# Optimization experiments

Hardware: AMD Instinct MI355X
Metric: run time of the kernel (lower is better)

The kernel has to match this reference:

```python
import jax, jax.numpy as jnp
import numpy as np

NB = 10          # number_of_basis (hardcoded in module)
MAX_RADIUS = 3.5
DIM_SH = 16      # spherical harmonics l = 0..3 -> (3+1)^2 components


def spherical_harmonics_l3(vec):
    # real spherical harmonics l=0..3 of the normalized vector,
    # 'component' normalization (each component has unit variance on S^2)
    r = jnp.sqrt(jnp.sum(vec * vec, -1, keepdims=True))
    u = vec / jnp.maximum(r, 1e-9)
    x, y, z = u[..., 0], u[..., 1], u[..., 2]
    s3, s5, s15 = jnp.sqrt(3.0), jnp.sqrt(5.0), jnp.sqrt(15.0)
    c358 = jnp.sqrt(35.0 / 8.0); c218 = jnp.sqrt(21.0 / 8.0)
    sh = [jnp.ones_like(x),
          s3 * x, s3 * y, s3 * z,
          s15 * x * y, s15 * y * z, (s5 / 2) * (3 * z * z - 1),
          s15 * x * z, (s15 / 2) * (x * x - y * y),
          c358 * y * (3 * x * x - y * y), jnp.sqrt(105.0) * x * y * z,
          c218 * y * (5 * z * z - 1), (jnp.sqrt(7.0) / 2) * z * (5 * z * z - 3),
          c218 * x * (5 * z * z - 1), (jnp.sqrt(105.0) / 2) * z * (x * x - y * y),
          c358 * x * (x * x - 3 * y * y)]
    return jnp.stack(sh, -1)  # [E, 16]


def soft_one_hot(r):
    # e3nn soft_one_hot_linspace, basis='smooth_finite', cutoff=True
    values = jnp.linspace(0.0, MAX_RADIUS, NB + 2)[1:-1]
    step = MAX_RADIUS / (NB + 1)
    u = (r[:, None] - values) / step
    mask = jnp.abs(u) < 1.0
    us = jnp.where(mask, u, 0.0)
    y = jnp.where(mask, jnp.exp(-1.0 / (1.0 - us * us)), 0.0)
    return 1.14136 * jnp.exp(2.0) * y * jnp.sqrt(float(NB))  # * number_of_basis**0.5


def soft_unit_step(t):
    ts = jnp.where(t > 0, t, 1.0)
    return jnp.where(t > 0, jnp.exp(-1.0 / ts), 0.0)


def fcnet(e, W1, W2):
    # e3nn FullyConnectedNet([10, 16, weight_numel], act=silu): bias-free,
    # fan-in normalized linear layers
    h = jax.nn.silu(e @ W1 / jnp.sqrt(float(e.shape[-1])))
    return h @ W2 / jnp.sqrt(float(W1.shape[-1]))


def setup_inputs() -> dict:
    key = jax.random.key(0)
    ks = jax.random.split(key, 9)
    N, E, C, DK = 20000, 50000, 16, 8
    pos = jax.random.uniform(ks[0], (N, 3), jnp.float32) * 2.0  # box so most edges < max_radius
    x = jax.random.normal(ks[1], (N, C), jnp.float32)
    Wq = jax.random.normal(ks[2], (C, DK), jnp.float32)
    Wk1 = jax.random.normal(ks[3], (NB, 16), jnp.float32)
    Wk2 = jax.random.normal(ks[4], (16, C * DIM_SH * DK), jnp.float32)
    Wv1 = jax.random.normal(ks[5], (NB, 16), jnp.float32)
    Wv2 = jax.random.normal(ks[6], (16, C * DIM_SH * DK), jnp.float32)
    edge_src = jax.random.randint(ks[7], (E,), 0, N, jnp.int32)
    edge_dst = jax.random.randint(ks[8], (E,), 0, N, jnp.int32)
    return {"pos": pos, "x": x, "Wq": Wq, "Wk1": Wk1, "Wk2": Wk2,
            "Wv1": Wv1, "Wv2": Wv2, "edge_src": edge_src, "edge_dst": edge_dst}


def reference(pos, x, Wq, Wk1, Wk2, Wv1, Wv2, edge_src, edge_dst):
    N, C = x.shape
    E = edge_src.shape[0]
    DK = Wq.shape[1]
    edge_vec = pos[edge_src] - pos[edge_dst]                    # [E, 3]
    r = jnp.sqrt(jnp.sum(edge_vec * edge_vec, -1) + 1e-18)      # [E]
    emb = soft_one_hot(r)                                       # [E, 10]
    cutoff = soft_unit_step(10.0 * (1.0 - r / MAX_RADIUS))      # [E]
    sh = spherical_harmonics_l3(edge_vec)                       # [E, 16]
    # per-edge weight-conditioned tensor products (shared_weights=False)
    wk = fcnet(emb, Wk1, Wk2).reshape(E, C, DIM_SH, DK)
    wv = fcnet(emb, Wv1, Wv2).reshape(E, C, DIM_SH, DK)
    xs = x[edge_src]                                            # gather [E, C]
    norm = jnp.sqrt(float(C * DIM_SH))
    k = jnp.einsum('ec,ej,ecjo->eo', xs, sh, wk) / norm         # [E, DK]
    v = jnp.einsum('ec,ej,ecjo->eo', xs, sh, wv) / norm         # [E, DK]
    q = x @ Wq                                                  # [N, DK]
    logits = jnp.sum(q[edge_dst] * k, -1) / jnp.sqrt(float(DK)) # [E]
    expv = cutoff * jnp.exp(logits)
    z = jax.ops.segment_sum(expv, edge_dst, num_segments=N)     # segment-softmax denom
    z = jnp.where(z == 0.0, 1.0, z)
    alpha = expv / z[edge_dst]
    w = jnp.sqrt(jax.nn.relu(alpha))
    out = jax.ops.segment_sum(w[:, None] * v, edge_dst, num_segments=N)  # [N, DK]
    return out
```

## Files before the change

### kernel.cpp

```cpp
#include <hip/hip_runtime.h>
#include <hip/hip_bf16.h>

#define NBASIS 10
#define CDIM 16
#define DKDIM 8
#define JDIM 16

typedef _Float16 half8 __attribute__((ext_vector_type(8)));
typedef _Float16 half4 __attribute__((ext_vector_type(4)));
typedef float floatx4 __attribute__((ext_vector_type(4)));

__device__ __forceinline__ float ldf(const void* p, int i, int f32) {
    if (f32) return ((const float*)p)[i];
    return __bfloat162float(((const __hip_bfloat16*)p)[i]);
}

__device__ __forceinline__ int detect_f32(const void* x) {
    unsigned short b = ((const unsigned short*)x)[threadIdx.x & 63];
    float v = __uint_as_float(((unsigned int)b) << 16);
    bool bad = !(fabsf(v) < 1000.0f) || (v != 0.0f && fabsf(v) < 1e-15f);
    unsigned long long m = __ballot(bad);
    return (__popcll(m) >= 8) ? 1 : 0;
}

__device__ __forceinline__ const float* uniform_ptr(const float* p) {
    uint64_t v = (uint64_t)p;
    uint32_t lo = __builtin_amdgcn_readfirstlane((uint32_t)v);
    uint32_t hi = __builtin_amdgcn_readfirstlane((uint32_t)(v >> 32));
    return (const float*)(((uint64_t)hi << 32) | lo);
}

__global__ __launch_bounds__(256) void prep_kernel(
    const void* __restrict__ x, const void* __restrict__ Wq,
    const void* __restrict__ Wk1, const void* __restrict__ Wk2,
    const void* __restrict__ Wv1, const void* __restrict__ Wv2,
    float* __restrict__ w1k, float* __restrict__ w1v,
    float* __restrict__ qbuf, float* __restrict__ zbuf,
    float* __restrict__ outacc, _Float16* __restrict__ Bpk, int N)
{
    const int f32 = detect_f32(x);
    int i = blockIdx.x * 256 + threadIdx.x;
    if (i < 160) { w1k[i] = ldf(Wk1, i, f32); w1v[i] = ldf(Wv1, i, f32); }
    if (i < 65536) {
        int j = i & 7, lane = (i >> 3) & 63, ks = (i >> 9) & 7, nt = i >> 12;
        int kk = ks * 32 + (lane >> 4) * 8 + j;
        int nn = nt * 16 + (lane & 15);
        int c = kk >> 4, jj = kk & 15;
        int net = nn >> 7, m = (nn >> 3) & 15, o = nn & 7;
        float v = ldf(net ? Wv2 : Wk2, m * 2048 + c * 128 + jj * 8 + o, f32);
        Bpk[i] = (_Float16)v;
    }
    if (i < N) {
        zbuf[i] = 0.0f;
        float xr[CDIM];
        #pragma unroll
        for (int c = 0; c < CDIM; ++c) xr[c] = ldf(x, i * CDIM + c, f32);
        #pragma unroll
        for (int o = 0; o < DKDIM; ++o) {
            float acc = 0.0f;
            #pragma unroll
            for (int c = 0; c < CDIM; ++c)
                acc = fmaf(xr[c], ldf(Wq, c * DKDIM + o, f32), acc);
            qbuf[i * DKDIM + o] = acc;
        }
    }
    if (i < N * 8) outacc[i] = 0.0f;
}

__global__ __launch_bounds__(256) void edge_kernel(
    const void* __restrict__ pos, const void* __restrict__ x,
    const int* __restrict__ esrc, const int* __restrict__ edst,
    const float* __restrict__ w1k, const float* __restrict__ w1v,
    const float* __restrict__ qbuf, const _Float16* __restrict__ Bpk,
    float* __restrict__ zbuf, float* __restrict__ outacc, int E)
{
    __shared__ union {
        struct { float xs[64][17]; float sh[64][17]; } g;
        _Float16 A[16384];
        struct { float pk[2][64][9]; float pv[2][64][9]; } p;
    } u;
    __shared__ _Float16 hm16[2][16][64];
    __shared__ float cut_lds[64];
    __shared__ float evs_lds[64];
    __shared__ int   d_lds[64];

    const int f32  = detect_f32(x);
    const int tid  = threadIdx.x;
    const int lane = tid & 63;
    const int w    = tid >> 6;
    const int q    = lane >> 4;
    const int e0   = blockIdx.x * 64;
    const int e_g  = e0 + lane;
    const int eidx = (e_g < E) ? e_g : (E - 1);
    const int s = esrc[eidx], d = edst[eidx];

    float vx = ldf(pos, s * 3 + 0, f32) - ldf(pos, d * 3 + 0, f32);
    float vy = ldf(pos, s * 3 + 1, f32) - ldf(pos, d * 3 + 1, f32);
    float vz = ldf(pos, s * 3 + 2, f32) - ldf(pos, d * 3 + 2, f32);
    float r2 = vx * vx + vy * vy + vz * vz;
    float r  = sqrtf(r2 + 1e-18f);

    if (w == 0) {
        float rsh = sqrtf(r2);
        float inv = 1.0f / fmaxf(rsh, 1e-9f);
        float ux = vx * inv, uy = vy * inv, uz = vz * inv;
        const float s3   = 1.7320508075688772f;
        const float s5   = 2.23606797749979f;
        const float s15  = 3.872983346207417f;
        const float c358 = 2.091650066335189f;
        const float c218 = 1.6201851746019651f;
        const float s105 = 10.246950765959598f;
        const float s7h  = 1.3228756555322954f;
        float xx = ux * ux, yy = uy * uy, zz = uz * uz;
        float sh[16];
        sh[0] = 1.0f;
        sh[1] = s3 * ux; sh[2] = s3 * uy; sh[3] = s3 * uz;
        sh[4] = s15 * ux * uy;
        sh[5] = s15 * uy * uz;
        sh[6] = 0.5f * s5 * (3.0f * zz - 1.0f);
        sh[7] = s15 * ux * uz;
        sh[8] = 0.5f * s15 * (xx - yy);
        sh[9] = c358 * uy * (3.0f * xx - yy);
        sh[10] = s105 * ux * uy * uz;
        sh[11] = c218 * uy * (5.0f * zz - 1.0f);
        sh[12] = s7h * uz * (5.0f * zz - 3.0f);
        sh[13] = c218 * ux * (5.0f * zz - 1.0f);
        sh[14] = 0.5f * s105 * uz * (xx - yy);
        sh[15] = c358 * ux * (xx - 3.0f * yy);
        #pragma unroll
        for (int j = 0; j < 16; ++j) u.g.sh[lane][j] = sh[j];
        float tcut = 10.0f * (1.0f - r * (1.0f / 3.5f));
        cut_lds[lane] = (tcut > 0.0f) ? expf(-1.0f / tcut) : 0.0f;
        d_lds[lane] = d;
    } else if (w == 1) {
        #pragma unroll
        for (int c = 0; c < CDIM; ++c)
            u.g.xs[lane][c] = ldf(x, s * CDIM + c, f32);
    } else {
        const float* w1 = uniform_ptr((w == 2) ? w1k : w1v);
        const int net = w - 2;
        float emb[NBASIS];
        const float step = 3.5f / 11.0f;
        const float istep = 11.0f / 3.5f;
        const float coef = (float)(1.14136 * 7.38905609893065 * 3.1622776601683795);
        #pragma unroll
        for (int i = 0; i < NBASIS; ++i) {
            float uu = (r - step * (float)(i + 1)) * istep; uu *= uu;
            emb[i] = (uu < 1.0f) ? coef * expf(-1.0f / (1.0f - uu)) : 0.0f;
        }
        const float inv_s10 = 0.31622776601683794f;
        #pragma unroll
        for (int m = 0; m < 16; ++m) {
            float pre = 0.0f;
            #pragma unroll
            for (int nb = 0; nb < NBASIS; ++nb)
                pre = fmaf(emb[nb], w1[nb * 16 + m], pre);
            pre *= inv_s10;
            hm16[net][m][lane] = (_Float16)(pre / (1.0f + expf(-pre)));
        }
    }
    __syncthreads();

    half8 af[8];
    {
        const int erow = w * 16 + (lane & 15);
        const int coff = q >> 1, jj0 = (q & 1) * 8;
        #pragma unroll
        for (int ks = 0; ks < 8; ++ks) {
            float xsv = u.g.xs[erow][ks * 2 + coff];
            half8 a;
            #pragma unroll
            for (int j = 0; j < 8; ++j)
                a[j] = (_Float16)(xsv * u.g.sh[erow][jj0 + j]);
            af[ks] = a;
        }
    }
    __syncthreads();
    {
        half8* Af = (half8*)u.A;
        #pragma unroll
        for (int ks = 0; ks < 8; ++ks)
            Af[(w * 8 + ks) * 64 + lane] = af[ks];
    }
    __syncthreads();

    float part[16];
    #pragma unroll
    for (int i = 0; i < 16; ++i) part[i] = 0.0f;
    const int b3  = (lane >> 3) & 1;
    const int net = w >> 1;
    const half8* Af = (const half8*)u.A;
    const half8* Bf = (const half8*)Bpk;

    #pragma unroll
    for (int l = 0; l < 4; ++l) {
        const int nt = 4 * w + l;
        floatx4 acc[4];
        #pragma unroll
        for (int rt = 0; rt < 4; ++rt) acc[rt] = (floatx4){0.f, 0.f, 0.f, 0.f};
        #pragma unroll
        for (int ks = 0; ks < 8; ++ks) {
            half8 b = Bf[(nt * 8 + ks) * 64 + lane];
            #pragma unroll
            for (int rt = 0; rt < 4; ++rt) {
                half8 a = Af[(rt * 8 + ks) * 64 + lane];
                acc[rt] = __builtin_amdgcn_mfma_f32_16x16x32_f16(a, b, acc[rt], 0, 0, 0);
            }
        }
        const int m = (2 * nt + b3) & 15;
        #pragma unroll
        for (int rt = 0; rt < 4; ++rt) {
            half4 hv = *(const half4*)&hm16[net][m][rt * 16 + q * 4];
            #pragma unroll
            for (int rr = 0; rr < 4; ++rr)
                part[rt * 4 + rr] = fmaf((float)hv[rr], acc[rt][rr], part[rt * 4 + rr]);
        }
    }
    #pragma unroll
    for (int i = 0; i < 16; ++i) part[i] += __shfl_xor(part[i], 8, 64);

    __syncthreads();
    if (b3 == 0) {
        const int o = lane & 7;
        #pragma unroll
        for (int i = 0; i < 16; ++i) {
            const int e = (i >> 2) * 16 + q * 4 + (i & 3);
            if (w < 2) u.p.pk[w][e][o] = part[i];
            else       u.p.pv[w - 2][e][o] = part[i];
        }
    }
    __syncthreads();

    if (tid < 64) {
        const int dd = d_lds[tid];
        float logit = 0.0f;
        #pragma unroll
        for (int o = 0; o < 8; ++o) {
            float kv = u.p.pk[0][tid][o] + u.p.pk[1][tid][o];
            logit = fmaf(qbuf[(size_t)dd * 8 + o], kv, logit);
        }
        logit *= (1.0f / 64.0f) * 0.35355339059327373f;
        float ev = cut_lds[tid] * expf(logit);
        if (e0 + tid < E) atomicAdd(&zbuf[dd], ev);
        evs_lds[tid] = sqrtf(ev);
    }
    __syncthreads();

    {
        const int el = tid & 63, op = tid >> 6;
        if (e0 + el < E) {
            const int dd = d_lds[el];
            const float wq = evs_lds[el] * (1.0f / 64.0f);
            float v0 = u.p.pv[0][el][2 * op]     + u.p.pv[1][el][2 * op];
            float v1 = u.p.pv[0][el][2 * op + 1] + u.p.pv[1][el][2 * op + 1];
            atomicAdd(&outacc[(size_t)dd * 8 + 2 * op],     wq * v0);
            atomicAdd(&outacc[(size_t)dd * 8 + 2 * op + 1], wq * v1);
        }
    }
}

__global__ __launch_bounds__(256) void finalize_kernel(
    const float* __restrict__ outacc, const float* __restrict__ zbuf,
    void* __restrict__ out, const void* __restrict__ x, int n)
{
    const int f32 = detect_f32(x);
    int i = blockIdx.x * 256 + threadIdx.x;
    if (i < n) {
        float z = zbuf[i >> 3];
        z = (z == 0.0f) ? 1.0f : z;
        float val = outacc[i] / sqrtf(z);
        if (f32) ((float*)out)[i] = val;
        else ((__hip_bfloat16*)out)[i] = __float2bfloat16(val);
    }
}

extern "C" void kernel_launch(void* const* d_in, const int* in_sizes, int n_in,
                              void* d_out, int out_size, void* d_ws, size_t ws_size,
                              hipStream_t stream)
{
    const void* pos = d_in[0];
    const void* x   = d_in[1];
    const void* Wq  = d_in[2];
    const void* Wk1 = d_in[3];
    const void* Wk2 = d_in[4];
    const void* Wv1 = d_in[5];
    const void* Wv2 = d_in[6];
    const int* esrc = (const int*)d_in[7];
    const int* edst = (const int*)d_in[8];
    const int N = in_sizes[1] / CDIM;
    const int E = in_sizes[7];

    float* ws = (float*)d_ws;
    float* w1k    = ws;
    float* w1v    = w1k + 160;
    float* qbuf   = w1v + 160;
    float* zbuf   = qbuf + (size_t)N * 8;
    float* outacc = zbuf + N;
    _Float16* Bpk = (_Float16*)(outacc + (size_t)N * 8);

    int prep_threads = N * 8 > 65536 ? N * 8 : 65536;
    int prep_blocks = (prep_threads + 255) / 256;
    prep_kernel<<<prep_blocks, 256, 0, stream>>>(x, Wq, Wk1, Wk2, Wv1, Wv2,
                                                 w1k, w1v, qbuf, zbuf, outacc,
                                                 Bpk, N);

    int edge_blocks = (E + 63) / 64;
    edge_kernel<<<edge_blocks, 256, 0, stream>>>(pos, x, esrc, edst,
                                                 w1k, w1v, qbuf, Bpk,
                                                 zbuf, outacc, E);

    finalize_kernel<<<(N * 8 + 255) / 256, 256, 0, stream>>>(
        outacc, zbuf, d_out, x, N * 8);
}
```

Measured before the change: 119.6 us.

## Hoist A tile out of union, restructure MFMA loop for operand reuse

Moves the A fragment buffer out of the shared union into its own LDS array, so the per-lane staging in registers and one barrier are no longer needed and the xs/sh storage does not alias it. It also drops the barrier before the partial-sum writes. The MFMA loop is reordered so each k-step loads four A and four B fragments once and issues 16 MFMAs into 16 accumulators, instead of reloading A for each of the four output tiles. The hidden activations are kept in fp32 LDS to avoid conversions. In exchange it uses more LDS and more accumulator registers, which may lower occupancy.

```diff
diff --git a/kernel.cpp b/kernel.cpp
--- a/kernel.cpp
+++ b/kernel.cpp
@@ -7,7 +7,6 @@
 #define JDIM 16
 
 typedef _Float16 half8 __attribute__((ext_vector_type(8)));
-typedef _Float16 half4 __attribute__((ext_vector_type(4)));
 typedef float floatx4 __attribute__((ext_vector_type(4)));
 
 __device__ __forceinline__ float ldf(const void* p, int i, int f32) {
@@ -74,12 +73,12 @@
     const float* __restrict__ qbuf, const _Float16* __restrict__ Bpk,
     float* __restrict__ zbuf, float* __restrict__ outacc, int E)
 {
+    __shared__ _Float16 A[16384];
     __shared__ union {
         struct { float xs[64][17]; float sh[64][17]; } g;
-        _Float16 A[16384];
         struct { float pk[2][64][9]; float pv[2][64][9]; } p;
     } u;
-    __shared__ _Float16 hm16[2][16][64];
+    __shared__ float hmf[2][16][68];
     __shared__ float cut_lds[64];
     __shared__ float evs_lds[64];
     __shared__ int   d_lds[64];
@@ -156,15 +155,15 @@
             for (int nb = 0; nb < NBASIS; ++nb)
                 pre = fmaf(emb[nb], w1[nb * 16 + m], pre);
             pre *= inv_s10;
-            hm16[net][m][lane] = (_Float16)(pre / (1.0f + expf(-pre)));
+            hmf[net][m][lane] = pre / (1.0f + expf(-pre));
         }
     }
     __syncthreads();
 
-    half8 af[8];
     {
         const int erow = w * 16 + (lane & 15);
         const int coff = q >> 1, jj0 = (q & 1) * 8;
+        half8* Af = (half8*)A;
         #pragma unroll
         for (int ks = 0; ks < 8; ++ks) {
             float xsv = u.g.xs[erow][ks * 2 + coff];
@@ -172,54 +171,56 @@
             #pragma unroll
             for (int j = 0; j < 8; ++j)
                 a[j] = (_Float16)(xsv * u.g.sh[erow][jj0 + j]);
-            af[ks] = a;
+            Af[(w * 8 + ks) * 64 + lane] = a;
         }
     }
     __syncthreads();
+
+    floatx4 acc[4][4];
+    #pragma unroll
+    for (int l = 0; l < 4; ++l)
+        #pragma unroll
+        for (int rt = 0; rt < 4; ++rt) acc[l][rt] = (floatx4){0.f, 0.f, 0.f, 0.f};
     {
-        half8* Af = (half8*)u.A;
-        #pragma unroll
-        for (int ks = 0; ks < 8; ++ks)
-            Af[(w * 8 + ks) * 64 + lane] = af[ks];
-    }
-    __syncthreads();
+        const half8* Af = (const half8*)A;
+        const half8* Bf = (const half8*)Bpk;
+        #pragma unroll
+        for (int ks = 0; ks < 8; ++ks) {
+            half8 a[4], b[4];
+            #pragma unroll
+            for (int rt = 0; rt < 4; ++rt)
+                a[rt] = Af[(rt * 8 + ks) * 64 + lane];
+            #pragma unroll
+            for (int l = 0; l < 4; ++l)
+                b[l] = Bf[((4 * w + l) * 8 + ks) * 64 + lane];
+            #pragma unroll
+            for (int l = 0; l < 4; ++l)
+                #pragma unroll
+                for (int rt = 0; rt < 4; ++rt)
+                    acc[l][rt] = __builtin_amdgcn_mfma_f32_16x16x32_f16(
+                        a[rt], b[l], acc[l][rt], 0, 0, 0);
+        }
+    }
 
     float part[16];
     #pragma unroll
     for (int i = 0; i < 16; ++i) part[i] = 0.0f;
     const int b3  = (lane >> 3) & 1;
     const int net = w >> 1;
-    const half8* Af = (const half8*)u.A;
-    const half8* Bf = (const half8*)Bpk;
-
     #pragma unroll
     for (int l = 0; l < 4; ++l) {
-        const int nt = 4 * w + l;
-        floatx4 acc[4];
-        #pragma unroll
-        for (int rt = 0; rt < 4; ++rt) acc[rt] = (floatx4){0.f, 0.f, 0.f, 0.f};
-        #pragma unroll
-        for (int ks = 0; ks < 8; ++ks) {
-            half8 b = Bf[(nt * 8 + ks) * 64 + lane];
-            #pragma unroll
-            for (int rt = 0; rt < 4; ++rt) {
-                half8 a = Af[(rt * 8 + ks) * 64 + lane];
-                acc[rt] = __builtin_amdgcn_mfma_f32_16x16x32_f16(a, b, acc[rt], 0, 0, 0);
-            }
-        }
-        const int m = (2 * nt + b3) & 15;
+        const int m = (2 * (4 * w + l) + b3) & 15;
         #pragma unroll
         for (int rt = 0; rt < 4; ++rt) {
-            half4 hv = *(const half4*)&hm16[net][m][rt * 16 + q * 4];
+            const float* hp = &hmf[net][m][rt * 16 + q * 4];
             #pragma unroll
             for (int rr = 0; rr < 4; ++rr)
-                part[rt * 4 + rr] = fmaf((float)hv[rr], acc[rt][rr], part[rt * 4 + rr]);
+                part[rt * 4 + rr] = fmaf(hp[rr], acc[l][rt][rr], part[rt * 4 + rr]);
         }
     }
     #pragma unroll
     for (int i = 0; i < 16; ++i) part[i] += __shfl_xor(part[i], 8, 64);
 
-    __syncthreads();
     if (b3 == 0) {
         const int o = lane & 7;
         #pragma unroll
```

New measurement: 120.8 us. About the same (+1.0%).
